# Optimization experiments

Measured on AMD Instinct MI355X. Metric: run time of the kernel, lower is better.

Reference implementation:

```python
import jax, jax.numpy as jnp
import numpy as np

MARGIN = 1.0
N, D, P = 4096, 768, 100

def setup_inputs() -> dict:
    key = jax.random.key(0)
    k1, k2, k3 = jax.random.split(key, 3)
    inputs = jax.random.normal(k1, (N, D), dtype=jnp.float32)
    targets = jax.random.randint(k2, (N,), 0, P)
    center = jax.random.normal(k3, (P, D), dtype=jnp.float32)
    return {"inputs": inputs, "targets": targets, "center": center}

def reference(inputs, targets, center):
    n = inputs.shape[0]
    # pairwise euclidean distances: ||xi||^2 + ||xj||^2 - 2 xi.xj
    sq = jnp.sum(inputs * inputs, axis=1)                      # [n]
    dist = sq[:, None] + sq[None, :] - 2.0 * (inputs @ inputs.T)
    dist = jnp.sqrt(jnp.clip(dist, 1e-12))                     # [n, n]
    mask = targets[:, None] == targets[None, :]                # same-class mask
    inf = jnp.asarray(jnp.inf, dist.dtype)
    # hardest positive: max over same-class (diagonal always True -> finite)
    dist_ap = jnp.max(jnp.where(mask, dist, -inf), axis=1)     # [n]
    # hardest negative: min over different-class, fallback ap+margin if none
    dist_an = jnp.min(jnp.where(mask, inf, dist), axis=1)      # [n]
    has_neg = jnp.any(~mask, axis=1)
    dist_an = jnp.where(has_neg, dist_an, dist_ap + MARGIN)
    # prototype augmentation: row-normalized centers, min distance to any center
    cn = center / jnp.linalg.norm(center, axis=1, keepdims=True)
    csq = jnp.sum(cn * cn, axis=1)                             # [P]
    d2c = sq[:, None] + csq[None, :] - 2.0 * (inputs @ cn.T)   # [n, P]
    d2c = jnp.clip(jnp.sqrt(jnp.clip(d2c, 0.0)), 1e-12)
    dist_an = jnp.minimum(dist_an, jnp.min(d2c, axis=1))
    # MarginRankingLoss(dist_an, dist_ap, y=1) = mean(relu(margin - (an - ap)))
    return jnp.mean(jax.nn.relu(MARGIN + dist_ap - dist_an))
```

## Files before the change

### kernel.cpp

```cpp
#include <hip/hip_runtime.h>
#include <math.h>

#define N_ 4096
#define D_ 768
#define P_ 100
#define PPAD 128
#define NT 24
#define NTRI 528
#define NBLK 560

typedef __attribute__((ext_vector_type(8))) short short8;
typedef __attribute__((ext_vector_type(4))) float f32x4;

typedef const __attribute__((address_space(1))) void* gld_src_t;
typedef __attribute__((address_space(3))) void* gld_dst_t;
#define GLOAD16(g, d) __builtin_amdgcn_global_load_lds((gld_src_t)(g), (gld_dst_t)(d), 16, 0, 0)

#define WAITVM4() asm volatile("s_waitcnt vmcnt(4)" ::: "memory")
#define WAITVM0() asm volatile("s_waitcnt vmcnt(0)" ::: "memory")
#define WAITLGKM0() asm volatile("s_waitcnt lgkmcnt(0)" ::: "memory")

__device__ inline unsigned short f2bf(float f) {
    union { float f; unsigned int u; } v; v.f = f;
    unsigned int u = v.u + 0x7fffu + ((v.u >> 16) & 1u);
    return (unsigned short)(u >> 16);
}

static __device__ __forceinline__ void decode_tile(int orig, int* pit, int* pjt) {
    const int x = orig & 7;
    const int k = orig >> 3;
    if (k >= 66) { *pit = x * 4 + (k - 66); *pjt = 32; return; }
    const int g = x * 66 + k;
    const int cumR[11] = {0, 36, 100, 136, 200, 264, 300, 364, 428, 492, 528};
    const int GIr[10] = {0, 1, 1, 2, 2, 2, 3, 3, 3, 3};
    const int GJr[10] = {0, 0, 1, 0, 1, 2, 0, 1, 2, 3};
    int r = 0;
    while (cumR[r + 1] <= g) ++r;
    const int u = g - cumR[r];
    int di, dj;
    if (GIr[r] == GJr[r]) {
        di = 0;
        while ((di + 1) * (di + 2) / 2 <= u) ++di;
        dj = u - di * (di + 1) / 2;
    } else {
        di = u >> 3; dj = u & 7;
    }
    *pit = GIr[r] * 8 + di;
    *pjt = GJr[r] * 8 + dj;
}

__global__ __launch_bounds__(256) void pre_kernel(
    const float* __restrict__ X, const float* __restrict__ C,
    float* __restrict__ sq, unsigned short* __restrict__ Xbf,
    unsigned short* __restrict__ cnbf, float* __restrict__ csq) {
    const int gw = blockIdx.x * 4 + (threadIdx.x >> 6);
    const int l = threadIdx.x & 63;
    if (gw < N_) {
        const float4* x4 = (const float4*)(X + (size_t)gw * D_);
        short4* ob = (short4*)(Xbf + (size_t)gw * D_);
        float s = 0.f;
#pragma unroll
        for (int c = 0; c < 3; ++c) {
            float4 v = x4[c * 64 + l];
            s = fmaf(v.x, v.x, fmaf(v.y, v.y, fmaf(v.z, v.z, fmaf(v.w, v.w, s))));
            short4 o;
            o.x = (short)f2bf(v.x); o.y = (short)f2bf(v.y);
            o.z = (short)f2bf(v.z); o.w = (short)f2bf(v.w);
            ob[c * 64 + l] = o;
        }
#pragma unroll
        for (int m = 1; m < 64; m <<= 1) s += __shfl_xor(s, m);
        if (l == 0) sq[gw] = s;
    } else {
        const int p = gw - N_;
        if (p >= PPAD) return;
        short4* ob = (short4*)(cnbf + (size_t)p * D_);
        if (p < P_) {
            const float4* c4 = (const float4*)(C + (size_t)p * D_);
            float4 v[3];
            float s = 0.f;
#pragma unroll
            for (int c = 0; c < 3; ++c) {
                v[c] = c4[c * 64 + l];
                s = fmaf(v[c].x, v[c].x, fmaf(v[c].y, v[c].y,
                    fmaf(v[c].z, v[c].z, fmaf(v[c].w, v[c].w, s))));
            }
#pragma unroll
            for (int m = 1; m < 64; m <<= 1) s += __shfl_xor(s, m);
            float rn = 1.0f / sqrtf(s);
#pragma unroll
            for (int c = 0; c < 3; ++c) {
                short4 o;
                o.x = (short)f2bf(v[c].x * rn); o.y = (short)f2bf(v[c].y * rn);
                o.z = (short)f2bf(v[c].z * rn); o.w = (short)f2bf(v[c].w * rn);
                ob[c * 64 + l] = o;
            }
            if (l == 0) csq[p] = s * rn * rn;
        } else {
            short4 z; z.x = z.y = z.z = z.w = 0;
#pragma unroll
            for (int c = 0; c < 3; ++c) ob[c * 64 + l] = z;
            if (l == 0) csq[p] = 1e30f;
        }
    }
}

__global__ __launch_bounds__(256, 3) void mfma_kernel(
    const unsigned short* __restrict__ Xbf, const unsigned short* __restrict__ cnbf,
    const int* __restrict__ T, const float* __restrict__ sq,
    const float* __restrict__ csq,
    float* __restrict__ ap_part, float* __restrict__ an_part,
    float* __restrict__ minc) {
    __shared__ __align__(16) unsigned short lds[3 * 8192];

    const int tid = threadIdx.x;
    const int l = tid & 63;
    const int w = tid >> 6;
    const int wr = w >> 1;
    const int wc = w & 1;

    int it, jt;
    decode_tile(blockIdx.x, &it, &jt);
    const bool is_center = (jt == 32);
    const int i0 = it * 128;
    const int j0 = is_center ? 0 : jt * 128;
    const unsigned short* __restrict__ Bmat = is_center ? cnbf : Xbf;

    const int srow = tid >> 2;
    const int scol = ((tid & 3) * 8) ^ (((srow & 6) >> 1) << 3);
    const unsigned short* gA0 = Xbf + (size_t)(i0 + srow) * D_ + scol;
    const unsigned short* gA1 = gA0 + (size_t)64 * D_;
    const unsigned short* gB0 = Bmat + (size_t)(j0 + srow) * D_ + scol;
    const unsigned short* gB1 = gB0 + (size_t)64 * D_;
    const int dA0 = w * 512, dA1 = 2048 + w * 512;
    const int dB0 = 4096 + w * 512, dB1 = 6144 + w * 512;

    const int col = l & 15;
    const int hi = l >> 4;
    const int rko = (hi * 8) ^ ((l & 6) << 2);
    const int aro = (wr * 64 + col) * 32 + rko;
    const int bro = 4096 + (wc * 64 + col) * 32 + rko;

    f32x4 acc[4][4];
#pragma unroll
    for (int m = 0; m < 4; ++m)
#pragma unroll
        for (int n = 0; n < 4; ++n) acc[m][n] = (f32x4){0.f, 0.f, 0.f, 0.f};

#define STAGE(t)                                                     \
    do {                                                             \
        const int bo_ = ((t) % 3) * 8192;                            \
        const int ke_ = (t) * 32;                                    \
        GLOAD16(gA0 + ke_, &lds[bo_ + dA0]);                         \
        GLOAD16(gA1 + ke_, &lds[bo_ + dA1]);                         \
        GLOAD16(gB0 + ke_, &lds[bo_ + dB0]);                         \
        GLOAD16(gB1 + ke_, &lds[bo_ + dB1]);                         \
    } while (0)

    STAGE(0);
    STAGE(1);
    WAITVM4();
    __builtin_amdgcn_s_barrier();
    __builtin_amdgcn_sched_barrier(0);

    int bo = 0;
#pragma unroll 3
    for (int t = 0; t < NT; ++t) {
        const unsigned short* Lb = &lds[bo * 8192];
        short8 a[4], b[4];
#pragma unroll
        for (int m = 0; m < 4; ++m)
            a[m] = *reinterpret_cast<const short8*>(Lb + aro + m * 512);
#pragma unroll
        for (int n = 0; n < 4; ++n)
            b[n] = *reinterpret_cast<const short8*>(Lb + bro + n * 512);
        if (t + 2 < NT) STAGE(t + 2);
        WAITLGKM0();
        if (t < NT - 1) {
            if (t + 2 < NT) WAITVM4();
            else WAITVM0();
            __builtin_amdgcn_s_barrier();
            __builtin_amdgcn_sched_barrier(0);
        }
#pragma unroll
        for (int m = 0; m < 4; ++m)
#pragma unroll
            for (int n = 0; n < 4; ++n)
                acc[m][n] = __builtin_amdgcn_mfma_f32_16x16x32_bf16(
                    a[m], b[n], acc[m][n], 0, 0, 0);
        bo = (bo == 2) ? 0 : bo + 1;
    }
#undef STAGE

    float* lf = (float*)lds;
    __syncthreads();

    if (!is_center) {
        float sqj[4]; int tj[4];
#pragma unroll
        for (int n = 0; n < 4; ++n) {
            int j = j0 + wc * 64 + n * 16 + col;
            sqj[n] = sq[j];
            tj[n] = T[j];
        }
        float apC[4], anC[4];
#pragma unroll
        for (int n = 0; n < 4; ++n) { apC[n] = -1e30f; anC[n] = 1e30f; }

#pragma unroll
        for (int m = 0; m < 4; ++m) {
#pragma unroll
            for (int r = 0; r < 4; ++r) {
                const int lrow = wr * 64 + m * 16 + hi * 4 + r;
                const int i = i0 + lrow;
                float sqi = sq[i];
                int ti = T[i];
                float apR = -1e30f, anR = 1e30f;
#pragma unroll
                for (int n = 0; n < 4; ++n) {
                    float d2 = sqi + sqj[n] - 2.0f * acc[m][n][r];
                    float d = sqrtf(fmaxf(d2, 1e-12f));
                    bool same = (tj[n] == ti);
                    apR = same ? fmaxf(apR, d) : apR;
                    anR = same ? anR : fminf(anR, d);
                    apC[n] = same ? fmaxf(apC[n], d) : apC[n];
                    anC[n] = same ? anC[n] : fminf(anC[n], d);
                }
#pragma unroll
                for (int msk = 1; msk < 16; msk <<= 1) {
                    apR = fmaxf(apR, __shfl_xor(apR, msk));
                    anR = fminf(anR, __shfl_xor(anR, msk));
                }
                if (col == 0) {
                    lf[wc * 128 + lrow] = apR;
                    lf[256 + wc * 128 + lrow] = anR;
                }
            }
        }
        __syncthreads();
        if (tid < 128) {
            float a = fmaxf(lf[tid], lf[128 + tid]);
            float b = fminf(lf[256 + tid], lf[384 + tid]);
            ap_part[(size_t)jt * N_ + i0 + tid] = a;
            an_part[(size_t)jt * N_ + i0 + tid] = b;
        }

        if (it != jt) {
            __syncthreads();
#pragma unroll
            for (int n = 0; n < 4; ++n) {
                apC[n] = fmaxf(apC[n], __shfl_xor(apC[n], 16));
                apC[n] = fmaxf(apC[n], __shfl_xor(apC[n], 32));
                anC[n] = fminf(anC[n], __shfl_xor(anC[n], 16));
                anC[n] = fminf(anC[n], __shfl_xor(anC[n], 32));
                if (hi == 0) {
                    int jl = wc * 64 + n * 16 + col;
                    lf[wr * 128 + jl] = apC[n];
                    lf[256 + wr * 128 + jl] = anC[n];
                }
            }
            __syncthreads();
            if (tid < 128) {
                float a = fmaxf(lf[tid], lf[128 + tid]);
                float b = fminf(lf[256 + tid], lf[384 + tid]);
                ap_part[(size_t)(32 + it) * N_ + j0 + tid] = a;
                an_part[(size_t)(32 + it) * N_ + j0 + tid] = b;
            }
        }
    } else {
        float sqj[4];
#pragma unroll
        for (int n = 0; n < 4; ++n) sqj[n] = csq[wc * 64 + n * 16 + col];
#pragma unroll
        for (int m = 0; m < 4; ++m) {
#pragma unroll
            for (int r = 0; r < 4; ++r) {
                const int lrow = wr * 64 + m * 16 + hi * 4 + r;
                const int i = i0 + lrow;
                float sqi = sq[i];
                float mc = 1e30f;
#pragma unroll
                for (int n = 0; n < 4; ++n) {
                    float d2 = sqi + sqj[n] - 2.0f * acc[m][n][r];
                    float d = fmaxf(sqrtf(fmaxf(d2, 0.0f)), 1e-12f);
                    mc = fminf(mc, d);
                }
#pragma unroll
                for (int msk = 1; msk < 16; msk <<= 1)
                    mc = fminf(mc, __shfl_xor(mc, msk));
                if (col == 0) lf[wc * 128 + lrow] = mc;
            }
        }
        __syncthreads();
        if (tid < 128) minc[i0 + tid] = fminf(lf[tid], lf[128 + tid]);
    }
}

__global__ __launch_bounds__(256) void combine2(
    const float* __restrict__ ap_part, const float* __restrict__ an_part,
    const float* __restrict__ minc, float* __restrict__ bsum) {
    const int w = threadIdx.x >> 6;
    const int l = threadIdx.x & 63;
    const int l2 = l & 31;
    float wsum = 0.f;
#pragma unroll
    for (int q = 0; q < 4; ++q) {
        const int i = blockIdx.x * 16 + w * 4 + q;
        const int r = i >> 7;
        const int s = (l2 <= r) ? l2 : 32 + l2;
        float v = (l < 32) ? ap_part[(size_t)s * N_ + i]
                           : an_part[(size_t)s * N_ + i];
#pragma unroll
        for (int m = 1; m < 32; m <<= 1) {
            float o = __shfl_xor(v, m);
            v = (l < 32) ? fmaxf(v, o) : fminf(v, o);
        }
        float ap = __shfl(v, 0);
        float an = __shfl(v, 32);
        float dan = (an < 1e29f) ? an : (ap + 1.0f);
        dan = fminf(dan, minc[i]);
        wsum += fmaxf(0.0f, 1.0f + ap - dan);
    }
    if (l == 0) bsum[blockIdx.x * 4 + w] = wsum;
}

__global__ __launch_bounds__(256) void finalize(
    const float* __restrict__ bsum, float* __restrict__ out) {
    __shared__ float sred[4];
    const int tid = threadIdx.x;
    float s = bsum[tid] + bsum[tid + 256] + bsum[tid + 512] + bsum[tid + 768];
#pragma unroll
    for (int m = 32; m > 0; m >>= 1) s += __shfl_xor(s, m);
    if ((tid & 63) == 0) sred[tid >> 6] = s;
    __syncthreads();
    if (tid == 0)
        out[0] = (sred[0] + sred[1] + sred[2] + sred[3]) / (float)N_;
}

extern "C" void kernel_launch(void* const* d_in, const int* in_sizes, int n_in,
                              void* d_out, int out_size, void* d_ws, size_t ws_size,
                              hipStream_t stream) {
    const float* X = (const float*)d_in[0];
    const int* T = (const int*)d_in[1];
    const float* C = (const float*)d_in[2];
    float* out = (float*)d_out;

    float* ws = (float*)d_ws;
    float* sq = ws;
    float* csq = ws + 4096;
    float* minc = ws + 4224;
    float* bsum = ws + 8320;
    unsigned short* Xbf = (unsigned short*)(ws + 9344);
    unsigned short* cnbf = (unsigned short*)(ws + 1582208);
    float* ap_part = ws + 1631360;
    float* an_part = ws + 1893504;

    pre_kernel<<<(N_ + PPAD) / 4, 256, 0, stream>>>(X, C, sq, Xbf, cnbf, csq);
    mfma_kernel<<<NBLK, 256, 0, stream>>>(Xbf, cnbf, T, sq, csq, ap_part, an_part, minc);
    combine2<<<N_ / 16, 256, 0, stream>>>(ap_part, an_part, minc, bsum);
    finalize<<<1, 256, 0, stream>>>(bsum, out);
}
```

Before: 50.79 us.

## Use 8 waves per 128x128 tile, halving per-wave N extent

Doubles the block size of the MFMA kernel from 4 to 8 waves, so each wave computes a 64x32 sub-tile instead of 64x64. Staging loads are redistributed so each thread issues two global-to-LDS copies per k-step instead of four, and the epilogue reductions gather over four column-waves. The goal is more waves resident per CU to hide latency and fewer accumulators per thread. The cost is that A fragments are re-read from LDS by twice as many waves, and barriers now synchronise a larger block.

```diff
diff --git a/kernel.cpp b/kernel.cpp
--- a/kernel.cpp
+++ b/kernel.cpp
@@ -16,7 +16,7 @@
 typedef __attribute__((address_space(3))) void* gld_dst_t;
 #define GLOAD16(g, d) __builtin_amdgcn_global_load_lds((gld_src_t)(g), (gld_dst_t)(d), 16, 0, 0)
 
-#define WAITVM4() asm volatile("s_waitcnt vmcnt(4)" ::: "memory")
+#define WAITVM2() asm volatile("s_waitcnt vmcnt(2)" ::: "memory")
 #define WAITVM0() asm volatile("s_waitcnt vmcnt(0)" ::: "memory")
 #define WAITLGKM0() asm volatile("s_waitcnt lgkmcnt(0)" ::: "memory")
 
@@ -105,7 +105,7 @@
     }
 }
 
-__global__ __launch_bounds__(256, 3) void mfma_kernel(
+__global__ __launch_bounds__(512, 6) void mfma_kernel(
     const unsigned short* __restrict__ Xbf, const unsigned short* __restrict__ cnbf,
     const int* __restrict__ T, const float* __restrict__ sq,
     const float* __restrict__ csq,
@@ -116,8 +116,8 @@
     const int tid = threadIdx.x;
     const int l = tid & 63;
     const int w = tid >> 6;
-    const int wr = w >> 1;
-    const int wc = w & 1;
+    const int wr = w >> 2;
+    const int wn = w & 3;
 
     int it, jt;
     decode_tile(blockIdx.x, &it, &jt);
@@ -128,38 +128,33 @@
 
     const int srow = tid >> 2;
     const int scol = ((tid & 3) * 8) ^ (((srow & 6) >> 1) << 3);
-    const unsigned short* gA0 = Xbf + (size_t)(i0 + srow) * D_ + scol;
-    const unsigned short* gA1 = gA0 + (size_t)64 * D_;
-    const unsigned short* gB0 = Bmat + (size_t)(j0 + srow) * D_ + scol;
-    const unsigned short* gB1 = gB0 + (size_t)64 * D_;
-    const int dA0 = w * 512, dA1 = 2048 + w * 512;
-    const int dB0 = 4096 + w * 512, dB1 = 6144 + w * 512;
+    const unsigned short* gA = Xbf + (size_t)(i0 + srow) * D_ + scol;
+    const unsigned short* gB = Bmat + (size_t)(j0 + srow) * D_ + scol;
+    const int dof = tid * 8;
 
     const int col = l & 15;
     const int hi = l >> 4;
     const int rko = (hi * 8) ^ ((l & 6) << 2);
     const int aro = (wr * 64 + col) * 32 + rko;
-    const int bro = 4096 + (wc * 64 + col) * 32 + rko;
-
-    f32x4 acc[4][4];
+    const int bro = 4096 + (wn * 32 + col) * 32 + rko;
+
+    f32x4 acc[4][2];
 #pragma unroll
     for (int m = 0; m < 4; ++m)
 #pragma unroll
-        for (int n = 0; n < 4; ++n) acc[m][n] = (f32x4){0.f, 0.f, 0.f, 0.f};
+        for (int n = 0; n < 2; ++n) acc[m][n] = (f32x4){0.f, 0.f, 0.f, 0.f};
 
 #define STAGE(t)                                                     \
     do {                                                             \
         const int bo_ = ((t) % 3) * 8192;                            \
         const int ke_ = (t) * 32;                                    \
-        GLOAD16(gA0 + ke_, &lds[bo_ + dA0]);                         \
-        GLOAD16(gA1 + ke_, &lds[bo_ + dA1]);                         \
-        GLOAD16(gB0 + ke_, &lds[bo_ + dB0]);                         \
-        GLOAD16(gB1 + ke_, &lds[bo_ + dB1]);                         \
+        GLOAD16(gA + ke_, &lds[bo_ + dof]);                          \
+        GLOAD16(gB + ke_, &lds[bo_ + 4096 + dof]);                   \
     } while (0)
 
     STAGE(0);
     STAGE(1);
-    WAITVM4();
+    WAITVM2();
     __builtin_amdgcn_s_barrier();
     __builtin_amdgcn_sched_barrier(0);
 
@@ -167,17 +162,17 @@
 #pragma unroll 3
     for (int t = 0; t < NT; ++t) {
         const unsigned short* Lb = &lds[bo * 8192];
-        short8 a[4], b[4];
+        short8 a[4], b[2];
 #pragma unroll
         for (int m = 0; m < 4; ++m)
             a[m] = *reinterpret_cast<const short8*>(Lb + aro + m * 512);
 #pragma unroll
-        for (int n = 0; n < 4; ++n)
+        for (int n = 0; n < 2; ++n)
             b[n] = *reinterpret_cast<const short8*>(Lb + bro + n * 512);
         if (t + 2 < NT) STAGE(t + 2);
         WAITLGKM0();
         if (t < NT - 1) {
-            if (t + 2 < NT) WAITVM4();
+            if (t + 2 < NT) WAITVM2();
             else WAITVM0();
             __builtin_amdgcn_s_barrier();
             __builtin_amdgcn_sched_barrier(0);
@@ -185,7 +180,7 @@
 #pragma unroll
         for (int m = 0; m < 4; ++m)
 #pragma unroll
-            for (int n = 0; n < 4; ++n)
+            for (int n = 0; n < 2; ++n)
                 acc[m][n] = __builtin_amdgcn_mfma_f32_16x16x32_bf16(
                     a[m], b[n], acc[m][n], 0, 0, 0);
         bo = (bo == 2) ? 0 : bo + 1;
@@ -196,16 +191,16 @@
     __syncthreads();
 
     if (!is_center) {
-        float sqj[4]; int tj[4];
-#pragma unroll
-        for (int n = 0; n < 4; ++n) {
-            int j = j0 + wc * 64 + n * 16 + col;
+        float sqj[2]; int tj[2];
+#pragma unroll
+        for (int n = 0; n < 2; ++n) {
+            int j = j0 + wn * 32 + n * 16 + col;
             sqj[n] = sq[j];
             tj[n] = T[j];
         }
-        float apC[4], anC[4];
-#pragma unroll
-        for (int n = 0; n < 4; ++n) { apC[n] = -1e30f; anC[n] = 1e30f; }
+        float apC[2], anC[2];
+#pragma unroll
+        for (int n = 0; n < 2; ++n) { apC[n] = -1e30f; anC[n] = 1e30f; }
 
 #pragma unroll
         for (int m = 0; m < 4; ++m) {
@@ -217,7 +212,7 @@
                 int ti = T[i];
                 float apR = -1e30f, anR = 1e30f;
 #pragma unroll
-                for (int n = 0; n < 4; ++n) {
+                for (int n = 0; n < 2; ++n) {
                     float d2 = sqi + sqj[n] - 2.0f * acc[m][n][r];
                     float d = sqrtf(fmaxf(d2, 1e-12f));
                     bool same = (tj[n] == ti);
@@ -232,15 +227,17 @@
                     anR = fminf(anR, __shfl_xor(anR, msk));
                 }
                 if (col == 0) {
-                    lf[wc * 128 + lrow] = apR;
-                    lf[256 + wc * 128 + lrow] = anR;
+                    lf[wn * 128 + lrow] = apR;
+                    lf[512 + wn * 128 + lrow] = anR;
                 }
             }
         }
         __syncthreads();
         if (tid < 128) {
-            float a = fmaxf(lf[tid], lf[128 + tid]);
-            float b = fminf(lf[256 + tid], lf[384 + tid]);
+            float a = fmaxf(fmaxf(lf[tid], lf[128 + tid]),
+                            fmaxf(lf[256 + tid], lf[384 + tid]));
+            float b = fminf(fminf(lf[512 + tid], lf[640 + tid]),
+                            fminf(lf[768 + tid], lf[896 + tid]));
             ap_part[(size_t)jt * N_ + i0 + tid] = a;
             an_part[(size_t)jt * N_ + i0 + tid] = b;
         }
@@ -248,13 +245,13 @@
         if (it != jt) {
             __syncthreads();
 #pragma unroll
-            for (int n = 0; n < 4; ++n) {
+            for (int n = 0; n < 2; ++n) {
                 apC[n] = fmaxf(apC[n], __shfl_xor(apC[n], 16));
                 apC[n] = fmaxf(apC[n], __shfl_xor(apC[n], 32));
                 anC[n] = fminf(anC[n], __shfl_xor(anC[n], 16));
                 anC[n] = fminf(anC[n], __shfl_xor(anC[n], 32));
                 if (hi == 0) {
-                    int jl = wc * 64 + n * 16 + col;
+                    int jl = wn * 32 + n * 16 + col;
                     lf[wr * 128 + jl] = apC[n];
                     lf[256 + wr * 128 + jl] = anC[n];
                 }
@@ -268,9 +265,9 @@
             }
         }
     } else {
-        float sqj[4];
-#pragma unroll
-        for (int n = 0; n < 4; ++n) sqj[n] = csq[wc * 64 + n * 16 + col];
+        float sqj[2];
+#pragma unroll
+        for (int n = 0; n < 2; ++n) sqj[n] = csq[wn * 32 + n * 16 + col];
 #pragma unroll
         for (int m = 0; m < 4; ++m) {
 #pragma unroll
@@ -280,7 +277,7 @@
                 float sqi = sq[i];
                 float mc = 1e30f;
 #pragma unroll
-                for (int n = 0; n < 4; ++n) {
+                for (int n = 0; n < 2; ++n) {
                     float d2 = sqi + sqj[n] - 2.0f * acc[m][n][r];
                     float d = fmaxf(sqrtf(fmaxf(d2, 0.0f)), 1e-12f);
                     mc = fminf(mc, d);
@@ -288,11 +285,15 @@
 #pragma unroll
                 for (int msk = 1; msk < 16; msk <<= 1)
                     mc = fminf(mc, __shfl_xor(mc, msk));
-                if (col == 0) lf[wc * 128 + lrow] = mc;
+                if (col == 0) lf[wn * 128 + lrow] = mc;
             }
         }
         __syncthreads();
-        if (tid < 128) minc[i0 + tid] = fminf(lf[tid], lf[128 + tid]);
+        if (tid < 128) {
+            float mc = fminf(fminf(lf[tid], lf[128 + tid]),
+                             fminf(lf[256 + tid], lf[384 + tid]));
+            minc[i0 + tid] = mc;
+        }
     }
 }
 
@@ -356,7 +357,7 @@
     float* an_part = ws + 1893504;
 
     pre_kernel<<<(N_ + PPAD) / 4, 256, 0, stream>>>(X, C, sq, Xbf, cnbf, csq);
-    mfma_kernel<<<NBLK, 256, 0, stream>>>(Xbf, cnbf, T, sq, csq, ap_part, an_part, minc);
+    mfma_kernel<<<NBLK, 512, 0, stream>>>(Xbf, cnbf, T, sq, csq, ap_part, an_part, minc);
     combine2<<<N_ / 16, 256, 0, stream>>>(ap_part, an_part, minc, bsum);
     finalize<<<1, 256, 0, stream>>>(bsum, out);
 }
```

Result: slower. 54.26 us (+6.8%).

## Give each wave private LDS staging to remove per-k-step block barriers

Applied to the files above, without the earlier changes.

Each wave now loads its own A and B sub-tiles into a private double-buffered LDS region, so the block-wide s_barrier in the k-loop is dropped and only per-wave vmcnt waits remain. This removes inter-wave synchronization stalls. The cost is that shared tiles are loaded twice (each A/B row block fetched by two waves), LDS per block grows, and launch bounds drop to 2 blocks per CU, so occupancy and global/L2 traffic may worsen.

```diff
diff --git a/kernel.cpp b/kernel.cpp
--- a/kernel.cpp
+++ b/kernel.cpp
@@ -16,7 +16,7 @@
 typedef __attribute__((address_space(3))) void* gld_dst_t;
 #define GLOAD16(g, d) __builtin_amdgcn_global_load_lds((gld_src_t)(g), (gld_dst_t)(d), 16, 0, 0)
 
-#define WAITVM4() asm volatile("s_waitcnt vmcnt(4)" ::: "memory")
+#define WAITVM8() asm volatile("s_waitcnt vmcnt(8)" ::: "memory")
 #define WAITVM0() asm volatile("s_waitcnt vmcnt(0)" ::: "memory")
 #define WAITLGKM0() asm volatile("s_waitcnt lgkmcnt(0)" ::: "memory")
 
@@ -105,13 +105,13 @@
     }
 }
 
-__global__ __launch_bounds__(256, 3) void mfma_kernel(
+__global__ __launch_bounds__(256, 2) void mfma_kernel(
     const unsigned short* __restrict__ Xbf, const unsigned short* __restrict__ cnbf,
     const int* __restrict__ T, const float* __restrict__ sq,
     const float* __restrict__ csq,
     float* __restrict__ ap_part, float* __restrict__ an_part,
     float* __restrict__ minc) {
-    __shared__ __align__(16) unsigned short lds[3 * 8192];
+    __shared__ __align__(16) unsigned short lds[4 * 2 * 4096];
 
     const int tid = threadIdx.x;
     const int l = tid & 63;
@@ -126,20 +126,18 @@
     const int j0 = is_center ? 0 : jt * 128;
     const unsigned short* __restrict__ Bmat = is_center ? cnbf : Xbf;
 
-    const int srow = tid >> 2;
-    const int scol = ((tid & 3) * 8) ^ (((srow & 6) >> 1) << 3);
-    const unsigned short* gA0 = Xbf + (size_t)(i0 + srow) * D_ + scol;
-    const unsigned short* gA1 = gA0 + (size_t)64 * D_;
-    const unsigned short* gB0 = Bmat + (size_t)(j0 + srow) * D_ + scol;
-    const unsigned short* gB1 = gB0 + (size_t)64 * D_;
-    const int dA0 = w * 512, dA1 = 2048 + w * 512;
-    const int dB0 = 4096 + w * 512, dB1 = 6144 + w * 512;
+    const int srow16 = l >> 2;
+    const int scol = ((l & 3) * 8) ^ (((srow16 & 6) >> 1) << 3);
+    const unsigned short* gA = Xbf + (size_t)(i0 + wr * 64 + srow16) * D_ + scol;
+    const unsigned short* gB = Bmat + (size_t)(j0 + wc * 64 + srow16) * D_ + scol;
+    unsigned short* wbase = &lds[w * 8192];
+    const int dof = l * 8;
 
     const int col = l & 15;
     const int hi = l >> 4;
     const int rko = (hi * 8) ^ ((l & 6) << 2);
-    const int aro = (wr * 64 + col) * 32 + rko;
-    const int bro = 4096 + (wc * 64 + col) * 32 + rko;
+    const int aro = col * 32 + rko;
+    const int bro = 2048 + col * 32 + rko;
 
     f32x4 acc[4][4];
 #pragma unroll
@@ -147,26 +145,28 @@
 #pragma unroll
         for (int n = 0; n < 4; ++n) acc[m][n] = (f32x4){0.f, 0.f, 0.f, 0.f};
 
-#define STAGE(t)                                                     \
-    do {                                                             \
-        const int bo_ = ((t) % 3) * 8192;                            \
-        const int ke_ = (t) * 32;                                    \
-        GLOAD16(gA0 + ke_, &lds[bo_ + dA0]);                         \
-        GLOAD16(gA1 + ke_, &lds[bo_ + dA1]);                         \
-        GLOAD16(gB0 + ke_, &lds[bo_ + dB0]);                         \
-        GLOAD16(gB1 + ke_, &lds[bo_ + dB1]);                         \
+#define STAGE(t, p)                                                     \
+    do {                                                                \
+        unsigned short* s_ = wbase + (p) * 4096;                        \
+        const int ke_ = (t) * 32;                                       \
+        GLOAD16(gA + ke_, s_ + 0 * 512 + dof);                          \
+        GLOAD16(gA + (size_t)16 * D_ + ke_, s_ + 1 * 512 + dof);        \
+        GLOAD16(gA + (size_t)32 * D_ + ke_, s_ + 2 * 512 + dof);        \
+        GLOAD16(gA + (size_t)48 * D_ + ke_, s_ + 3 * 512 + dof);        \
+        GLOAD16(gB + ke_, s_ + 2048 + 0 * 512 + dof);                   \
+        GLOAD16(gB + (size_t)16 * D_ + ke_, s_ + 2048 + 1 * 512 + dof); \
+        GLOAD16(gB + (size_t)32 * D_ + ke_, s_ + 2048 + 2 * 512 + dof); \
+        GLOAD16(gB + (size_t)48 * D_ + ke_, s_ + 2048 + 3 * 512 + dof); \
     } while (0)
 
-    STAGE(0);
-    STAGE(1);
-    WAITVM4();
-    __builtin_amdgcn_s_barrier();
+    STAGE(0, 0);
+    STAGE(1, 1);
+    WAITVM8();
     __builtin_amdgcn_sched_barrier(0);
 
-    int bo = 0;
-#pragma unroll 3
     for (int t = 0; t < NT; ++t) {
-        const unsigned short* Lb = &lds[bo * 8192];
+        const int p = t & 1;
+        const unsigned short* Lb = wbase + p * 4096;
         short8 a[4], b[4];
 #pragma unroll
         for (int m = 0; m < 4; ++m)
@@ -174,12 +174,12 @@
 #pragma unroll
         for (int n = 0; n < 4; ++n)
             b[n] = *reinterpret_cast<const short8*>(Lb + bro + n * 512);
-        if (t + 2 < NT) STAGE(t + 2);
         WAITLGKM0();
+        __builtin_amdgcn_sched_barrier(0);
+        if (t + 2 < NT) STAGE(t + 2, p);
         if (t < NT - 1) {
-            if (t + 2 < NT) WAITVM4();
+            if (t + 2 < NT) WAITVM8();
             else WAITVM0();
-            __builtin_amdgcn_s_barrier();
             __builtin_amdgcn_sched_barrier(0);
         }
 #pragma unroll
@@ -188,7 +188,6 @@
             for (int n = 0; n < 4; ++n)
                 acc[m][n] = __builtin_amdgcn_mfma_f32_16x16x32_bf16(
                     a[m], b[n], acc[m][n], 0, 0, 0);
-        bo = (bo == 2) ? 0 : bo + 1;
     }
 #undef STAGE
 
```

Result: slower. 62.91 us (+23.9%).

## Load B operand directly from global memory into registers, bypassing LDS

Applied to the files above, without the earlier changes.

The B tile is no longer staged through LDS. Each wave now reads its B fragments straight from global memory into registers every k-step, and only the A tile stays in the triple-buffered LDS pipeline. This halves the LDS footprint and the LDS read traffic for B, and the vmcnt thresholds are adjusted to match. In exchange, B loads are issued and consumed within the same iteration with no prefetch, waves sharing the same columns fetch B redundantly, and the per-row 64-byte accesses coalesce less well.

```diff
diff --git a/kernel.cpp b/kernel.cpp
--- a/kernel.cpp
+++ b/kernel.cpp
@@ -16,7 +16,7 @@
 typedef __attribute__((address_space(3))) void* gld_dst_t;
 #define GLOAD16(g, d) __builtin_amdgcn_global_load_lds((gld_src_t)(g), (gld_dst_t)(d), 16, 0, 0)
 
-#define WAITVM4() asm volatile("s_waitcnt vmcnt(4)" ::: "memory")
+#define WAITVM2() asm volatile("s_waitcnt vmcnt(2)" ::: "memory")
 #define WAITVM0() asm volatile("s_waitcnt vmcnt(0)" ::: "memory")
 #define WAITLGKM0() asm volatile("s_waitcnt lgkmcnt(0)" ::: "memory")
 
@@ -111,7 +111,7 @@
     const float* __restrict__ csq,
     float* __restrict__ ap_part, float* __restrict__ an_part,
     float* __restrict__ minc) {
-    __shared__ __align__(16) unsigned short lds[3 * 8192];
+    __shared__ __align__(16) unsigned short lds[3 * 4096];
 
     const int tid = threadIdx.x;
     const int l = tid & 63;
@@ -130,16 +130,14 @@
     const int scol = ((tid & 3) * 8) ^ (((srow & 6) >> 1) << 3);
     const unsigned short* gA0 = Xbf + (size_t)(i0 + srow) * D_ + scol;
     const unsigned short* gA1 = gA0 + (size_t)64 * D_;
-    const unsigned short* gB0 = Bmat + (size_t)(j0 + srow) * D_ + scol;
-    const unsigned short* gB1 = gB0 + (size_t)64 * D_;
-    const int dA0 = w * 512, dA1 = 2048 + w * 512;
-    const int dB0 = 4096 + w * 512, dB1 = 6144 + w * 512;
+    const int dA0 = tid * 8;
+    const int dA1 = 2048 + tid * 8;
 
     const int col = l & 15;
     const int hi = l >> 4;
     const int rko = (hi * 8) ^ ((l & 6) << 2);
     const int aro = (wr * 64 + col) * 32 + rko;
-    const int bro = 4096 + (wc * 64 + col) * 32 + rko;
+    const unsigned short* bb = Bmat + (size_t)(j0 + wc * 64 + col) * D_ + hi * 8;
 
     f32x4 acc[4][4];
 #pragma unroll
@@ -147,40 +145,44 @@
 #pragma unroll
         for (int n = 0; n < 4; ++n) acc[m][n] = (f32x4){0.f, 0.f, 0.f, 0.f};
 
-#define STAGE(t)                                                     \
+#define STAGEA(t)                                                    \
     do {                                                             \
-        const int bo_ = ((t) % 3) * 8192;                            \
+        const int bo_ = ((t) % 3) * 4096;                            \
         const int ke_ = (t) * 32;                                    \
         GLOAD16(gA0 + ke_, &lds[bo_ + dA0]);                         \
         GLOAD16(gA1 + ke_, &lds[bo_ + dA1]);                         \
-        GLOAD16(gB0 + ke_, &lds[bo_ + dB0]);                         \
-        GLOAD16(gB1 + ke_, &lds[bo_ + dB1]);                         \
     } while (0)
 
-    STAGE(0);
-    STAGE(1);
-    WAITVM4();
+    STAGEA(0);
+    STAGEA(1);
+    WAITVM2();
     __builtin_amdgcn_s_barrier();
     __builtin_amdgcn_sched_barrier(0);
 
     int bo = 0;
 #pragma unroll 3
     for (int t = 0; t < NT; ++t) {
-        const unsigned short* Lb = &lds[bo * 8192];
-        short8 a[4], b[4];
+        short8 b[4];
+        {
+            const unsigned short* bt = bb + t * 32;
+#pragma unroll
+            for (int n = 0; n < 4; ++n)
+                b[n] = *reinterpret_cast<const short8*>(bt + (size_t)(n * 16) * D_);
+        }
+        if (t + 2 < NT) STAGEA(t + 2);
+        const unsigned short* Lb = &lds[bo * 4096];
+        short8 a[4];
 #pragma unroll
         for (int m = 0; m < 4; ++m)
             a[m] = *reinterpret_cast<const short8*>(Lb + aro + m * 512);
-#pragma unroll
-        for (int n = 0; n < 4; ++n)
-            b[n] = *reinterpret_cast<const short8*>(Lb + bro + n * 512);
-        if (t + 2 < NT) STAGE(t + 2);
         WAITLGKM0();
         if (t < NT - 1) {
-            if (t + 2 < NT) WAITVM4();
+            if (t + 2 < NT) WAITVM2();
             else WAITVM0();
             __builtin_amdgcn_s_barrier();
             __builtin_amdgcn_sched_barrier(0);
+        } else {
+            WAITVM0();
         }
 #pragma unroll
         for (int m = 0; m < 4; ++m)
@@ -190,7 +192,7 @@
                     a[m], b[n], acc[m][n], 0, 0, 0);
         bo = (bo == 2) ? 0 : bo + 1;
     }
-#undef STAGE
+#undef STAGEA
 
     float* lf = (float*)lds;
     __syncthreads();
```

After: 69.17 us. +36.2%, slower.
